# Kernel tuning notes

Hardware: AMD Instinct MI355X
Metric: run time of the kernel (lower is better)

The kernel has to match this reference:

```python
import jax, jax.numpy as jnp
import numpy as np

N_NODES = 100000
N_EDGES = 1700000  # 1.6M random edges + 100k self-loops (dgl.add_self_loop)
HID = 128
N_GRAPHS = 64
N_CLASSES = 10
T_STEPS = 5


def setup_inputs() -> dict:
    key = jax.random.key(0)
    ks = jax.random.split(key, 12)
    m = jax.random.normal(ks[0], (N_NODES,), dtype=jnp.float32)
    n_rand = N_EDGES - N_NODES
    src_r = jax.random.randint(ks[1], (n_rand,), 0, N_NODES)
    dst_r = jax.random.randint(ks[2], (n_rand,), 0, N_NODES)
    loops = jnp.arange(N_NODES)
    src = jnp.concatenate([src_r, loops])
    dst = jnp.concatenate([dst_r, loops])
    graph_ids = jnp.sort(jax.random.randint(ks[3], (N_NODES,), 0, N_GRAPHS))
    s = 0.05
    W_e = jax.random.normal(ks[4], (HID, HID), dtype=jnp.float32) * s
    b_e = jnp.zeros((HID,), dtype=jnp.float32)
    W_ih = jax.random.normal(ks[5], (3 * HID, HID), dtype=jnp.float32) * s
    b_ih = jnp.zeros((3 * HID,), dtype=jnp.float32)
    W_hh = jax.random.normal(ks[6], (3 * HID, HID), dtype=jnp.float32) * s
    b_hh = jnp.zeros((3 * HID,), dtype=jnp.float32)
    W_cls = jax.random.normal(ks[7], (N_CLASSES, HID), dtype=jnp.float32) * s
    b_cls = jnp.zeros((N_CLASSES,), dtype=jnp.float32)
    return {"m": m, "W_e": W_e, "b_e": b_e, "W_ih": W_ih, "b_ih": b_ih,
            "W_hh": W_hh, "b_hh": b_hh, "W_cls": W_cls, "b_cls": b_cls,
            "src": src, "dst": dst, "graph_ids": graph_ids, "n_graphs": N_GRAPHS}


def _gated_graph_forward(m, W_e, b_e, W_ih, b_ih, W_hh, b_hh, W_cls, b_cls,
                         src, dst, graph_ids, n_graphs):
    n_nodes = m.shape[0]
    hid = W_e.shape[0]
    # h = ndata['m'].view(-1,1), zero-padded to out_feats (DGL GatedGraphConv)
    h = jnp.zeros((n_nodes, hid), dtype=m.dtype).at[:, 0].set(m)
    for _ in range(T_STEPS):
        # single edge type: a[v] = sum_{(u,v) in E} W_e h[u] + b_e
        msg = (h @ W_e.T + b_e)[src]                       # [E, H]
        a = jax.ops.segment_sum(msg, dst, num_segments=n_nodes)
        # torch.nn.GRUCell(a, h); gate order: r, z, n
        gi = a @ W_ih.T + b_ih
        gh = h @ W_hh.T + b_hh
        i_r, i_z, i_n = jnp.split(gi, 3, axis=-1)
        h_r, h_z, h_n = jnp.split(gh, 3, axis=-1)
        r = jax.nn.sigmoid(i_r + h_r)
        z = jax.nn.sigmoid(i_z + h_z)
        n = jnp.tanh(i_n + r * h_n)
        h = (1.0 - z) * n + z * h
    h = jax.nn.relu(h)
    # dgl.mean_nodes: per-graph mean over nodes
    sums = jax.ops.segment_sum(h, graph_ids, num_segments=n_graphs)
    cnt = jax.ops.segment_sum(jnp.ones((n_nodes,), h.dtype), graph_ids,
                              num_segments=n_graphs)
    hg = sums / jnp.maximum(cnt, 1.0)[:, None]             # [G, H]
    return hg @ W_cls.T + b_cls                            # [G, C]


def reference(m, W_e, b_e, W_ih, b_ih, W_hh, b_hh, W_cls, b_cls,
              src, dst, graph_ids, n_graphs):
    return _gated_graph_forward(m, W_e, b_e, W_ih, b_ih, W_hh, b_hh,
                                W_cls, b_cls, src, dst, graph_ids, n_graphs)
```

## Files before the change

kernel.cpp:

```cpp
#include <hip/hip_runtime.h>

#define HID 128
#define G3  384
#define TSTEPS 5
#define BSHIFT 9
#define BNODES (1 << BSHIFT)
#define MAXBUK 256
#define PART_EPB 8192

typedef unsigned int  uint;
typedef unsigned short ushort;

typedef float  f32x4  __attribute__((ext_vector_type(4)));
typedef __bf16 bf16x8 __attribute__((ext_vector_type(8)));

union B8u { uint4 u; bf16x8 b; ushort s[8]; };

static __device__ inline ushort f2bf(float f) {
  uint u = __float_as_uint(f);
  uint r = u + 0x7fffu + ((u >> 16) & 1u);
  return (ushort)(r >> 16);
}
static __device__ inline float bf2f(ushort s) {
  return __uint_as_float(((uint)s) << 16);
}

__global__ __launch_bounds__(128) void k_weights(
    const float* __restrict__ W_e, const float* __restrict__ b_e,
    const float* __restrict__ W_ih, const float* __restrict__ W_hh,
    ushort* __restrict__ Wcomb, ushort* __restrict__ Whh16, float* __restrict__ bvec)
{
  int j = blockIdx.x, t = threadIdx.x;
  if (j < G3) {
    __shared__ float row[HID];
    row[t] = W_ih[j * HID + t];
    __syncthreads();
    float acc = 0.f;
    for (int k = 0; k < HID; ++k) acc = fmaf(row[k], W_e[k * HID + t], acc);
    Wcomb[j * HID + t] = f2bf(acc);
    if (t == 0) {
      float b = 0.f;
      for (int k = 0; k < HID; ++k) b += row[k] * b_e[k];
      bvec[j] = b;
    }
  } else {
    int j2 = j - G3;
    Whh16[j2 * HID + t] = f2bf(W_hh[j2 * HID + t]);
  }
}

__global__ __launch_bounds__(256) void k_bh(const int* __restrict__ dst,
                                            int* __restrict__ bhist, int E) {
  __shared__ int lh[MAXBUK];
  int t = threadIdx.x;
  if (t < MAXBUK) lh[t] = 0;
  __syncthreads();
  for (int e = blockIdx.x * 256 + t; e < E; e += gridDim.x * 256)
    atomicAdd(&lh[dst[e] >> BSHIFT], 1);
  __syncthreads();
  if (t < MAXBUK && lh[t]) atomicAdd(&bhist[t], lh[t]);
}

__global__ __launch_bounds__(256) void k_bsc(const int* __restrict__ bhist,
                                             int* __restrict__ bbase,
                                             int* __restrict__ gcur,
                                             int* __restrict__ rowptr, int E, int N) {
  __shared__ int ls[MAXBUK];
  int t = threadIdx.x;
  ls[t] = bhist[t];
  __syncthreads();
  if (t == 0) {
    int run = 0;
    for (int i = 0; i < MAXBUK; ++i) {
      bbase[i] = run; gcur[i] = run; run += ls[i];
    }
    bbase[MAXBUK] = run;
    rowptr[N] = E;
  }
}

__global__ __launch_bounds__(256) void k_part(
    const int* __restrict__ src, const int* __restrict__ dst,
    int* __restrict__ gcur, uint* __restrict__ ebuf, int E) {
  __shared__ int lh[MAXBUK], lbase[MAXBUK], lcur[MAXBUK];
  int t = threadIdx.x;
  int base = blockIdx.x * PART_EPB;
  if (t < MAXBUK) lh[t] = 0;
  __syncthreads();
#pragma unroll 4
  for (int j = 0; j < PART_EPB / 256; ++j) {
    int e = base + j * 256 + t;
    if (e < E) atomicAdd(&lh[dst[e] >> BSHIFT], 1);
  }
  __syncthreads();
  if (t < MAXBUK) {
    lbase[t] = lh[t] ? atomicAdd(&gcur[t], lh[t]) : 0;
    lcur[t] = 0;
  }
  __syncthreads();
#pragma unroll 4
  for (int j = 0; j < PART_EPB / 256; ++j) {
    int e = base + j * 256 + t;
    if (e < E) {
      int d = dst[e];
      int b = d >> BSHIFT;
      int p = atomicAdd(&lcur[b], 1);
      ebuf[lbase[b] + p] = (uint)src[e] | ((uint)(d & (BNODES - 1)) << 20);
    }
  }
}

__global__ __launch_bounds__(256) void k_fill2(
    const uint* __restrict__ ebuf, const int* __restrict__ bbase,
    int* __restrict__ csrc, int* __restrict__ rowptr, int* __restrict__ deg, int N) {
  __shared__ int hcnt[BNODES];
  __shared__ int wls[4];
  int t = threadIdx.x;
  int b = blockIdx.x;
  int ebeg = bbase[b], eend = bbase[b + 1];
  for (int i = t; i < BNODES; i += 256) hcnt[i] = 0;
  __syncthreads();
  for (int e = ebeg + t; e < eend; e += 256)
    atomicAdd(&hcnt[ebuf[e] >> 20], 1);
  __syncthreads();
  const int PER = BNODES / 256;
  int lane = t & 63, wv = t >> 6;
  int x[PER]; int s = 0;
#pragma unroll
  for (int i = 0; i < PER; ++i) { x[i] = hcnt[PER * t + i]; s += x[i]; }
  int incl = s;
#pragma unroll
  for (int off = 1; off < 64; off <<= 1) {
    int u = __shfl_up(incl, off, 64);
    if (lane >= off) incl += u;
  }
  if (lane == 63) wls[wv] = incl;
  __syncthreads();
  int wbase = 0;
  for (int i = 0; i < wv; ++i) wbase += wls[i];
  int run = wbase + incl - s;
#pragma unroll
  for (int i = 0; i < PER; ++i) {
    int node = (b << BSHIFT) + PER * t + i;
    hcnt[PER * t + i] = run;
    if (node < N) { rowptr[node] = ebeg + run; deg[node] = x[i]; }
    run += x[i];
  }
  __syncthreads();
  for (int e = ebeg + t; e < eend; e += 256) {
    uint v = ebuf[e];
    int p = atomicAdd(&hcnt[v >> 20], 1);
    csrc[ebeg + p] = (int)(v & 0xFFFFFu);
  }
}

__global__ void k_init(const float* __restrict__ m, ushort* __restrict__ hb, int N) {
  int idx = blockIdx.x * 256 + threadIdx.x;
  if (idx >= N * HID) return;
  int d = idx & (HID - 1);
  float v = (d == 0) ? m[idx >> 7] : 0.f;
  hb[idx] = f2bf(v);
}

__global__ __launch_bounds__(256) void k_gather(
    const int* __restrict__ rowptr, const int* __restrict__ csrc,
    const ushort* __restrict__ hb, ushort* __restrict__ hs16, int N, int nstrip)
{
  int x = blockIdx.x & 7;
  int ii = blockIdx.x >> 3;
  int s = 8 * (ii >> 2) + x;
  if (s >= nstrip) return;
  int v = s * 16 + (ii & 3) * 4 + (threadIdx.x >> 6);
  if (v >= N) return;
  int lane = threadIdx.x & 63;
  int g = lane >> 4;
  int i = lane & 15;
  int beg = rowptr[v], end = rowptr[v + 1];
  float acc[8] = {0.f, 0.f, 0.f, 0.f, 0.f, 0.f, 0.f, 0.f};
  int e = beg;
  for (; e + 16 <= end; e += 16) {
    int s0 = csrc[e + g];
    int s1 = csrc[e + 4 + g];
    int s2 = csrc[e + 8 + g];
    int s3 = csrc[e + 12 + g];
    B8u w0; w0.u = *(const uint4*)(hb + (size_t)s0 * HID + i * 8);
    B8u w1; w1.u = *(const uint4*)(hb + (size_t)s1 * HID + i * 8);
    B8u w2; w2.u = *(const uint4*)(hb + (size_t)s2 * HID + i * 8);
    B8u w3; w3.u = *(const uint4*)(hb + (size_t)s3 * HID + i * 8);
#pragma unroll
    for (int j = 0; j < 8; ++j)
      acc[j] += (bf2f(w0.s[j]) + bf2f(w1.s[j])) + (bf2f(w2.s[j]) + bf2f(w3.s[j]));
  }
  for (; e < end; e += 4) {
    int ee = e + g;
    if (ee < end) {
      int s0 = csrc[ee];
      B8u w; w.u = *(const uint4*)(hb + (size_t)s0 * HID + i * 8);
#pragma unroll
      for (int j = 0; j < 8; ++j) acc[j] += bf2f(w.s[j]);
    }
  }
#pragma unroll
  for (int j = 0; j < 8; ++j) {
    acc[j] += __shfl_xor(acc[j], 16, 64);
    acc[j] += __shfl_xor(acc[j], 32, 64);
  }
  if (g == 0) {
    uint4 ov;
    ov.x = ((uint)f2bf(acc[1]) << 16) | (uint)f2bf(acc[0]);
    ov.y = ((uint)f2bf(acc[3]) << 16) | (uint)f2bf(acc[2]);
    ov.z = ((uint)f2bf(acc[5]) << 16) | (uint)f2bf(acc[4]);
    ov.w = ((uint)f2bf(acc[7]) << 16) | (uint)f2bf(acc[6]);
    *(uint4*)(hs16 + (size_t)v * HID + i * 8) = ov;
  }
}

struct GruCtx {
  const ushort* hs16; const ushort* hbc; ushort* hbn; const int* deg;
  int l16, quad, d;
  float bir, biz, bin_, bhr, bhz, bhn, vr, vz, vn;
};

static __device__ __forceinline__ void gru_load(
    const GruCtx& c, int s, B8u af[4], B8u hf[4], float hold[4], float degf[4]) {
  int n0 = s << 4;
  size_t arow = (size_t)(n0 + c.l16) * HID + c.quad * 8;
#pragma unroll
  for (int kc = 0; kc < 4; ++kc) {
    af[kc].u = *(const uint4*)(c.hs16 + arow + kc * 32);
    hf[kc].u = *(const uint4*)(c.hbc + arow + kc * 32);
  }
#pragma unroll
  for (int rg = 0; rg < 4; ++rg) {
    int n = n0 + c.quad * 4 + rg;
    hold[rg] = bf2f(c.hbc[(size_t)n * HID + c.d]);
    degf[rg] = (float)c.deg[n];
  }
}

static __device__ __forceinline__ void gru_compute(
    const GruCtx& c, int s, const B8u af[4], const B8u hf[4],
    const float hold[4], const float degf[4],
    const B8u bw[3][4], const B8u bh[3][4]) {
  f32x4 acc[6] = {};
#pragma unroll
  for (int kc = 0; kc < 4; ++kc)
#pragma unroll
    for (int g = 0; g < 3; ++g) {
      acc[g]     = __builtin_amdgcn_mfma_f32_16x16x32_bf16(af[kc].b, bw[g][kc].b, acc[g], 0, 0, 0);
      acc[3 + g] = __builtin_amdgcn_mfma_f32_16x16x32_bf16(hf[kc].b, bh[g][kc].b, acc[3 + g], 0, 0, 0);
    }
  int n0 = s << 4;
#pragma unroll
  for (int rg = 0; rg < 4; ++rg) {
    float ir = acc[0][rg] + degf[rg] * c.vr + c.bir;
    float iz = acc[1][rg] + degf[rg] * c.vz + c.biz;
    float in_ = acc[2][rg] + degf[rg] * c.vn + c.bin_;
    float hr = acc[3][rg] + c.bhr;
    float hz = acc[4][rg] + c.bhz;
    float hn = acc[5][rg] + c.bhn;
    float r = __builtin_amdgcn_rcpf(1.f + __expf(-(ir + hr)));
    float z = __builtin_amdgcn_rcpf(1.f + __expf(-(iz + hz)));
    float x2 = in_ + r * hn;
    float e2 = __expf(2.f * x2);
    float nv = 1.f - 2.f * __builtin_amdgcn_rcpf(e2 + 1.f);
    float hv = (1.f - z) * nv + z * hold[rg];
    c.hbn[(size_t)(n0 + c.quad * 4 + rg) * HID + c.d] = f2bf(hv);
  }
}

__global__ __launch_bounds__(512, 2) void k_gru(
    const ushort* __restrict__ hs16,
    const ushort* __restrict__ hbc, ushort* __restrict__ hbn,
    const ushort* __restrict__ Wcomb, const ushort* __restrict__ Whh16,
    const float* __restrict__ bvec, const float* __restrict__ b_ih,
    const float* __restrict__ b_hh, const int* __restrict__ deg, int N)
{
  const int w = threadIdx.x >> 6;
  const int lane = threadIdx.x & 63;
  const int quad = lane >> 4, l16 = lane & 15;
  const int d0 = w * 16;
  const int d = d0 + l16;

  B8u bw[3][4], bh[3][4];
#pragma unroll
  for (int g = 0; g < 3; ++g)
#pragma unroll
    for (int kc = 0; kc < 4; ++kc) {
      int j = (d0 + g * 128 + l16) * HID + kc * 32 + quad * 8;
      bw[g][kc].u = *(const uint4*)(Wcomb + j);
      bh[g][kc].u = *(const uint4*)(Whh16 + j);
    }

  GruCtx c;
  c.hs16 = hs16; c.hbc = hbc; c.hbn = hbn; c.deg = deg;
  c.l16 = l16; c.quad = quad; c.d = d;
  c.bir = b_ih[d]; c.biz = b_ih[d + 128]; c.bin_ = b_ih[d + 256];
  c.bhr = b_hh[d]; c.bhz = b_hh[d + 128]; c.bhn = b_hh[d + 256];
  c.vr = bvec[d]; c.vz = bvec[d + 128]; c.vn = bvec[d + 256];

  const int nstrip = N >> 4;
  const int G = (int)gridDim.x;
  int s = blockIdx.x;
  if (s >= nstrip) return;

  B8u afA[4], hfA[4], afB[4], hfB[4];
  float holdA[4], degA[4], holdB[4], degB[4];
  gru_load(c, s, afA, hfA, holdA, degA);

  while (true) {
    int ns = s + G;
    bool more = ns < nstrip;
    if (more) gru_load(c, ns, afB, hfB, holdB, degB);
    gru_compute(c, s, afA, hfA, holdA, degA, bw, bh);
    if (!more) break;
    s = ns;
    ns = s + G;
    more = ns < nstrip;
    if (more) gru_load(c, ns, afA, hfA, holdA, degA);
    gru_compute(c, s, afB, hfB, holdB, degB, bw, bh);
    if (!more) break;
    s = ns;
  }
}

__global__ __launch_bounds__(64) void k_bounds(const int* __restrict__ gid,
                                               int* __restrict__ cnt, int N, int G) {
  int g = threadIdx.x;
  if (g >= G) return;
  int lo = 0, hi = N;
  while (lo < hi) { int mid = (lo + hi) >> 1; if (gid[mid] < g) lo = mid + 1; else hi = mid; }
  int lb0 = lo;
  lo = 0; hi = N;
  int g1 = g + 1;
  while (lo < hi) { int mid = (lo + hi) >> 1; if (gid[mid] < g1) lo = mid + 1; else hi = mid; }
  cnt[g] = lo - lb0;
}

#define POOL_CHUNK 96
__global__ __launch_bounds__(128) void k_pool(const ushort* __restrict__ hb,
                                              const int* __restrict__ gid,
                                              float* __restrict__ hg, int N) {
  int d = threadIdx.x;
  int start = blockIdx.x * POOL_CHUNK;
  if (start >= N) return;
  int end = min(start + POOL_CHUNK, N);
  float acc = 0.f;
  int g = gid[start];
  for (int n = start; n < end; ++n) {
    int gn = gid[n];
    if (gn != g) { unsafeAtomicAdd(&hg[g * HID + d], acc); acc = 0.f; g = gn; }
    acc += fmaxf(bf2f(hb[(size_t)n * HID + d]), 0.f);
  }
  unsafeAtomicAdd(&hg[g * HID + d], acc);
}

__global__ __launch_bounds__(640) void k_cls(const float* __restrict__ hg,
                                             const int* __restrict__ cnt,
                                             const float* __restrict__ Wc,
                                             const float* __restrict__ bc,
                                             float* __restrict__ out, int G) {
  int t = threadIdx.x;
  if (t >= G * 10) return;
  int g = t / 10, c = t % 10;
  float inv = 1.f / fmaxf((float)cnt[g], 1.f);
  float acc = 0.f;
  for (int d = 0; d < HID; ++d) acc = fmaf(hg[g * HID + d], Wc[c * HID + d], acc);
  out[t] = acc * inv + bc[c];
}

extern "C" void kernel_launch(void* const* d_in, const int* in_sizes, int n_in,
                              void* d_out, int out_size, void* d_ws, size_t ws_size,
                              hipStream_t stream) {
  const int N = in_sizes[0];
  const int E = in_sizes[9];
  const float* m    = (const float*)d_in[0];
  const float* W_e  = (const float*)d_in[1];
  const float* b_e  = (const float*)d_in[2];
  const float* W_ih = (const float*)d_in[3];
  const float* b_ih = (const float*)d_in[4];
  const float* W_hh = (const float*)d_in[5];
  const float* b_hh = (const float*)d_in[6];
  const float* W_cls = (const float*)d_in[7];
  const float* b_cls = (const float*)d_in[8];
  const int* src = (const int*)d_in[9];
  const int* dst = (const int*)d_in[10];
  const int* gid = (const int*)d_in[11];
  const int G = out_size / 10;
  float* out = (float*)d_out;

  size_t off = 0;
  auto alloc = [&](size_t b) {
    char* p = (char*)d_ws + off;
    off += (b + 255) & ~(size_t)255;
    return (void*)p;
  };
  ushort* hb0    = (ushort*)alloc((size_t)N * HID * 2);
  ushort* hb1    = (ushort*)alloc((size_t)N * HID * 2);
  ushort* hs16   = (ushort*)alloc((size_t)N * HID * 2);
  int*    deg    = (int*)   alloc((size_t)N * 4);
  int*    rowptr = (int*)   alloc((size_t)(N + 1) * 4);
  int*    csrc   = (int*)   alloc((size_t)E * 4);
  uint*   ebuf   = (uint*)  alloc((size_t)E * 4);
  int*    bhist  = (int*)   alloc((size_t)MAXBUK * 4);
  int*    bbase  = (int*)   alloc((size_t)(MAXBUK + 1) * 4);
  int*    gcur   = (int*)   alloc((size_t)MAXBUK * 4);
  ushort* Wcomb  = (ushort*)alloc((size_t)G3 * HID * 2);
  ushort* Whh16  = (ushort*)alloc((size_t)G3 * HID * 2);
  float*  bvec   = (float*) alloc((size_t)G3 * 4);
  float*  hg     = (float*) alloc((size_t)G * HID * 4);
  int*    cnt    = (int*)   alloc((size_t)G * 4);
  if (off > ws_size) return;

  const int NBUK = (N + BNODES - 1) >> BSHIFT;

  k_weights<<<2 * G3, HID, 0, stream>>>(W_e, b_e, W_ih, W_hh, Wcomb, Whh16, bvec);
  hipMemsetAsync(bhist, 0, (size_t)MAXBUK * 4, stream);
  k_bh<<<256, 256, 0, stream>>>(dst, bhist, E);
  k_bsc<<<1, MAXBUK, 0, stream>>>(bhist, bbase, gcur, rowptr, E, N);
  k_part<<<(E + PART_EPB - 1) / PART_EPB, 256, 0, stream>>>(src, dst, gcur, ebuf, E);
  k_fill2<<<NBUK, 256, 0, stream>>>(ebuf, bbase, csrc, rowptr, deg, N);
  k_init<<<(N * HID + 255) / 256, 256, 0, stream>>>(m, hb0, N);

  ushort* hbc = hb0;
  ushort* hbn = hb1;
  const int nstrip = N >> 4;
  const int gather_blocks = 8 * ((nstrip + 7) / 8) * 4;
  const int gru_blocks = nstrip < 1024 ? nstrip : 1024;
  for (int s = 0; s < TSTEPS; ++s) {
    k_gather<<<gather_blocks, 256, 0, stream>>>(rowptr, csrc, hbc, hs16, N, nstrip);
    k_gru<<<gru_blocks, 512, 0, stream>>>(hs16, hbc, hbn, Wcomb, Whh16, bvec, b_ih, b_hh, deg, N);
    ushort* t = hbc; hbc = hbn; hbn = t;
  }

  hipMemsetAsync(hg, 0, (size_t)G * HID * 4, stream);
  k_bounds<<<1, 64, 0, stream>>>(gid, cnt, N, G);
  k_pool<<<(N + POOL_CHUNK - 1) / POOL_CHUNK, HID, 0, stream>>>(hbc, gid, hg, N);
  k_cls<<<1, 640, 0, stream>>>(hg, cnt, W_cls, b_cls, out, G);
}
```

Measured before the change: 932.9 us.

## Specialize first GGNN step using rank-one initial hidden state

Because the initial hidden state has only column 0 nonzero, the first step's message aggregation reduces to a scalar per-node neighbor sum of m, and the GRU matmuls reduce to outer products with column 0 of the combined and recurrent weights. New kernels compute the scalar gather and an elementwise GRU for step zero, replacing the full 128-wide gather and GEMM-based GRU for that step. This removes one full-width gather and GEMM pass but adds two small kernels and extra weight column extraction.

```diff
diff --git a/kernel.cpp b/kernel.cpp
--- a/kernel.cpp
+++ b/kernel.cpp
@@ -28,7 +28,8 @@
 __global__ __launch_bounds__(128) void k_weights(
     const float* __restrict__ W_e, const float* __restrict__ b_e,
     const float* __restrict__ W_ih, const float* __restrict__ W_hh,
-    ushort* __restrict__ Wcomb, ushort* __restrict__ Whh16, float* __restrict__ bvec)
+    ushort* __restrict__ Wcomb, ushort* __restrict__ Whh16, float* __restrict__ bvec,
+    ushort* __restrict__ Wc0, ushort* __restrict__ Wh0)
 {
   int j = blockIdx.x, t = threadIdx.x;
   if (j < G3) {
@@ -39,6 +40,7 @@
     for (int k = 0; k < HID; ++k) acc = fmaf(row[k], W_e[k * HID + t], acc);
     Wcomb[j * HID + t] = f2bf(acc);
     if (t == 0) {
+      Wc0[j] = f2bf(acc);
       float b = 0.f;
       for (int k = 0; k < HID; ++k) b += row[k] * b_e[k];
       bvec[j] = b;
@@ -46,6 +48,7 @@
   } else {
     int j2 = j - G3;
     Whh16[j2 * HID + t] = f2bf(W_hh[j2 * HID + t]);
+    if (t == 0) Wh0[j2] = f2bf(W_hh[j2 * HID]);
   }
 }
 
@@ -154,12 +157,72 @@
   }
 }
 
-__global__ void k_init(const float* __restrict__ m, ushort* __restrict__ hb, int N) {
+__global__ void k_minit(const float* __restrict__ m, ushort* __restrict__ m16, int N) {
+  int v = blockIdx.x * 256 + threadIdx.x;
+  if (v < N) m16[v] = f2bf(m[v]);
+}
+
+__global__ __launch_bounds__(256) void k_gather0(
+    const int* __restrict__ rowptr, const int* __restrict__ csrc,
+    const ushort* __restrict__ m16, ushort* __restrict__ hsum0, int N)
+{
+  int v = blockIdx.x * 256 + threadIdx.x;
+  if (v >= N) return;
+  int beg = rowptr[v], end = rowptr[v + 1];
+  float a0 = 0.f, a1 = 0.f, a2 = 0.f, a3 = 0.f;
+  int e = beg;
+  for (; e + 16 <= end; e += 16) {
+    a0 += (bf2f(m16[csrc[e + 0]]) + bf2f(m16[csrc[e + 4]])) +
+          (bf2f(m16[csrc[e + 8]]) + bf2f(m16[csrc[e + 12]]));
+    a1 += (bf2f(m16[csrc[e + 1]]) + bf2f(m16[csrc[e + 5]])) +
+          (bf2f(m16[csrc[e + 9]]) + bf2f(m16[csrc[e + 13]]));
+    a2 += (bf2f(m16[csrc[e + 2]]) + bf2f(m16[csrc[e + 6]])) +
+          (bf2f(m16[csrc[e + 10]]) + bf2f(m16[csrc[e + 14]]));
+    a3 += (bf2f(m16[csrc[e + 3]]) + bf2f(m16[csrc[e + 7]])) +
+          (bf2f(m16[csrc[e + 11]]) + bf2f(m16[csrc[e + 15]]));
+  }
+  for (; e < end; e += 4) {
+    if (e + 0 < end) a0 += bf2f(m16[csrc[e + 0]]);
+    if (e + 1 < end) a1 += bf2f(m16[csrc[e + 1]]);
+    if (e + 2 < end) a2 += bf2f(m16[csrc[e + 2]]);
+    if (e + 3 < end) a3 += bf2f(m16[csrc[e + 3]]);
+  }
+  hsum0[v] = f2bf((a0 + a1) + (a2 + a3));
+}
+
+__global__ __launch_bounds__(256) void k_gru0(
+    const ushort* __restrict__ hsum0, const ushort* __restrict__ m16,
+    const int* __restrict__ deg,
+    const ushort* __restrict__ Wc0, const ushort* __restrict__ Wh0,
+    const float* __restrict__ bvec, const float* __restrict__ b_ih,
+    const float* __restrict__ b_hh, ushort* __restrict__ hbn, int N)
+{
   int idx = blockIdx.x * 256 + threadIdx.x;
   if (idx >= N * HID) return;
-  int d = idx & (HID - 1);
-  float v = (d == 0) ? m[idx >> 7] : 0.f;
-  hb[idx] = f2bf(v);
+  int n = idx >> 7, d = idx & (HID - 1);
+  float s0 = bf2f(hsum0[n]);
+  float h0 = bf2f(m16[n]);
+  float degf = (float)deg[n];
+  float acc0 = s0 * bf2f(Wc0[d]);
+  float acc1 = s0 * bf2f(Wc0[d + 128]);
+  float acc2 = s0 * bf2f(Wc0[d + 256]);
+  float acc3 = h0 * bf2f(Wh0[d]);
+  float acc4 = h0 * bf2f(Wh0[d + 128]);
+  float acc5 = h0 * bf2f(Wh0[d + 256]);
+  float hold = (d == 0) ? h0 : 0.f;
+  float ir = acc0 + degf * bvec[d] + b_ih[d];
+  float iz = acc1 + degf * bvec[d + 128] + b_ih[d + 128];
+  float in_ = acc2 + degf * bvec[d + 256] + b_ih[d + 256];
+  float hr = acc3 + b_hh[d];
+  float hz = acc4 + b_hh[d + 128];
+  float hn = acc5 + b_hh[d + 256];
+  float r = __builtin_amdgcn_rcpf(1.f + __expf(-(ir + hr)));
+  float z = __builtin_amdgcn_rcpf(1.f + __expf(-(iz + hz)));
+  float x2 = in_ + r * hn;
+  float e2 = __expf(2.f * x2);
+  float nv = 1.f - 2.f * __builtin_amdgcn_rcpf(e2 + 1.f);
+  float hv = (1.f - z) * nv + z * hold;
+  hbn[idx] = f2bf(hv);
 }
 
 __global__ __launch_bounds__(256) void k_gather(
@@ -410,24 +473,32 @@
   float*  bvec   = (float*) alloc((size_t)G3 * 4);
   float*  hg     = (float*) alloc((size_t)G * HID * 4);
   int*    cnt    = (int*)   alloc((size_t)G * 4);
+  ushort* m16    = (ushort*)alloc((size_t)N * 2);
+  ushort* hsum0  = (ushort*)alloc((size_t)N * 2);
+  ushort* Wc0    = (ushort*)alloc((size_t)G3 * 2);
+  ushort* Wh0    = (ushort*)alloc((size_t)G3 * 2);
   if (off > ws_size) return;
 
   const int NBUK = (N + BNODES - 1) >> BSHIFT;
 
-  k_weights<<<2 * G3, HID, 0, stream>>>(W_e, b_e, W_ih, W_hh, Wcomb, Whh16, bvec);
+  k_weights<<<2 * G3, HID, 0, stream>>>(W_e, b_e, W_ih, W_hh, Wcomb, Whh16, bvec, Wc0, Wh0);
+  k_minit<<<(N + 255) / 256, 256, 0, stream>>>(m, m16, N);
   hipMemsetAsync(bhist, 0, (size_t)MAXBUK * 4, stream);
   k_bh<<<256, 256, 0, stream>>>(dst, bhist, E);
   k_bsc<<<1, MAXBUK, 0, stream>>>(bhist, bbase, gcur, rowptr, E, N);
   k_part<<<(E + PART_EPB - 1) / PART_EPB, 256, 0, stream>>>(src, dst, gcur, ebuf, E);
   k_fill2<<<NBUK, 256, 0, stream>>>(ebuf, bbase, csrc, rowptr, deg, N);
-  k_init<<<(N * HID + 255) / 256, 256, 0, stream>>>(m, hb0, N);
-
-  ushort* hbc = hb0;
-  ushort* hbn = hb1;
+
+  k_gather0<<<(N + 255) / 256, 256, 0, stream>>>(rowptr, csrc, m16, hsum0, N);
+  k_gru0<<<(N * HID + 255) / 256, 256, 0, stream>>>(hsum0, m16, deg, Wc0, Wh0,
+                                                    bvec, b_ih, b_hh, hb1, N);
+
+  ushort* hbc = hb1;
+  ushort* hbn = hb0;
   const int nstrip = N >> 4;
   const int gather_blocks = 8 * ((nstrip + 7) / 8) * 4;
   const int gru_blocks = nstrip < 1024 ? nstrip : 1024;
-  for (int s = 0; s < TSTEPS; ++s) {
+  for (int s = 1; s < TSTEPS; ++s) {
     k_gather<<<gather_blocks, 256, 0, stream>>>(rowptr, csrc, hbc, hs16, N, nstrip);
     k_gru<<<gru_blocks, 512, 0, stream>>>(hs16, hbc, hbn, Wcomb, Whh16, bvec, b_ih, b_hh, deg, N);
     ushort* t = hbc; hbc = hbn; hbn = t;
```

New measurement: 826.4 us. -11.4%, faster.
